# Performance work log

Hardware: AMD Instinct MI355X
Metric: run time of the kernel (lower is better)

## Reference

```python
import jax, jax.numpy as jnp
import numpy as np
from jax import lax

B = 128
ROUTING_ITER = 3
EPS = 1e-9


def _conv(x, w, b, stride):
    y = lax.conv_general_dilated(x, w, window_strides=(stride, stride), padding='VALID',
                                 dimension_numbers=('NCHW', 'OIHW', 'NCHW'))
    return y + b[None, :, None, None]


def _squash(s):
    # squash along capsule dim (axis=3), s: [B,1,10,16,1]
    sq = jnp.sum(s * s, axis=3, keepdims=True)
    return (sq / (1.0 + sq)) * s / jnp.sqrt(sq + EPS)


def setup_inputs() -> dict:
    key = jax.random.key(0)
    ks = jax.random.split(key, 16)
    x = jax.random.normal(ks[0], (B, 1, 28, 28), dtype=jnp.float32)
    labels = jax.random.randint(ks[1], (B,), 0, 10)
    y = jax.nn.one_hot(labels, 10, dtype=jnp.float32)
    conv1_w = jax.random.normal(ks[2], (256, 1, 9, 9), dtype=jnp.float32) * 0.05
    conv1_b = jnp.zeros((256,), dtype=jnp.float32)
    caps1_w = jax.random.normal(ks[3], (256, 256, 9, 9), dtype=jnp.float32) * 0.01
    caps1_b = jnp.zeros((256,), dtype=jnp.float32)
    W = jax.random.normal(ks[4], (1, 1152, 10, 8, 16), dtype=jnp.float32) * 0.05
    caps_bias = jnp.zeros((1, 1, 10, 16, 1), dtype=jnp.float32)
    fc1_w = jax.random.normal(ks[5], (512, 16), dtype=jnp.float32) * 0.1
    fc1_b = jnp.zeros((512,), dtype=jnp.float32)
    fc2_w = jax.random.normal(ks[6], (1024, 512), dtype=jnp.float32) * 0.04
    fc2_b = jnp.zeros((1024,), dtype=jnp.float32)
    fc3_w = jax.random.normal(ks[7], (784, 1024), dtype=jnp.float32) * 0.03
    fc3_b = jnp.zeros((784,), dtype=jnp.float32)
    return {'x': x, 'y': y, 'conv1_w': conv1_w, 'conv1_b': conv1_b,
            'caps1_w': caps1_w, 'caps1_b': caps1_b, 'W': W, 'caps_bias': caps_bias,
            'fc1_w': fc1_w, 'fc1_b': fc1_b, 'fc2_w': fc2_w, 'fc2_b': fc2_b,
            'fc3_w': fc3_w, 'fc3_b': fc3_b}


def _forward(x, y, conv1_w, conv1_b, caps1_w, caps1_b, W, caps_bias,
             fc1_w, fc1_b, fc2_w, fc2_b, fc3_w, fc3_b):
    h = jax.nn.relu(_conv(x, conv1_w, conv1_b, 1))          # [B,256,20,20]
    h = jax.nn.relu(_conv(h, caps1_w, caps1_b, 2))          # [B,256,6,6]

    # faithful repeat+view layout from the torch code (NOT a transpose)
    x_view = jnp.tile(h.reshape(B, 256, 1, 6, 6), (1, 1, 10, 1, 1)).reshape(B, 1152, 10, 8, 1)
    W_view = jnp.broadcast_to(W, (B, 1152, 10, 8, 16)).reshape(B, 1152, 10, 16, 8)
    u_hat = jnp.matmul(W_view, x_view)                      # [B,1152,10,16,1]
    u_hat_stopped = lax.stop_gradient(u_hat)

    b_ij = jnp.zeros((B, 1152, 10, 1, 1), dtype=u_hat.dtype)
    V_J = None
    for r in range(ROUTING_ITER):
        c_ij = jax.nn.softmax(b_ij, axis=2)                 # softmax over 10 classes
        if r < ROUTING_ITER - 1:
            s_j = jnp.sum(c_ij * u_hat_stopped, axis=1, keepdims=True) + caps_bias
            v_j = _squash(s_j)                              # [B,1,10,16,1]
            # agreement: u_hat^T . v, [B,1152,10,1,16] @ [B,1152,10,16,1]
            agree = jnp.matmul(u_hat_stopped.reshape(B, 1152, 10, 1, 16),
                               jnp.broadcast_to(v_j, (B, 1152, 10, 16, 1)))
            b_ij = b_ij + agree
        else:
            s_j = jnp.sum(c_ij * u_hat, axis=1, keepdims=True) + caps_bias
            V_J = _squash(s_j)                              # [B,1,10,16,1]

    caps_out = jnp.squeeze(V_J, axis=1)                     # [B,10,16,1]
    v_length = jnp.sqrt(jnp.sum(caps_out * caps_out, axis=2, keepdims=True) + EPS)
    v_length = v_length.reshape(B, 10, 1, 1)

    # torch: squeeze -> [B,10,16], then .view(B,16,10) (reshape, not transpose)
    flat = caps_out.reshape(B, 10, 16).reshape(B, 16, 10)
    masked_v = jnp.matmul(flat, y.reshape(B, 10, 1)).reshape(B, 16)

    fc1 = masked_v @ fc1_w.T + fc1_b                        # no activation (faithful)
    fc2 = fc1 @ fc2_w.T + fc2_b
    reconstruction = jax.nn.sigmoid(fc2 @ fc3_w.T + fc3_b)  # [B,784]
    return v_length, reconstruction


def reference(x, y, conv1_w, conv1_b, caps1_w, caps1_b, W, caps_bias,
              fc1_w, fc1_b, fc2_w, fc2_b, fc3_w, fc3_b):
    return _forward(x, y, conv1_w, conv1_b, caps1_w, caps1_b, W, caps_bias,
                    fc1_w, fc1_b, fc2_w, fc2_b, fc3_w, fc3_b)
```

## Files before the change

### kernel.cpp

```cpp
#include <hip/hip_runtime.h>
#include <hip/hip_bf16.h>

typedef unsigned short ushort_t;
typedef __attribute__((ext_vector_type(8))) short short8;
typedef __attribute__((ext_vector_type(4))) float f32x4;


#define OFFB_H1T  0u
#define OFFB_WT   26214400u
#define OFFB_PART 36831232u
#define OFFB_H2   55705600u
#define OFFB_UH   60424192u
#define OFFB_BIJ  107610112u
#define OFFB_C    113508352u
#define OFFB_V    119406592u
#define OFFB_F1   119488512u
#define OFFB_F2   119750656u

__device__ __forceinline__ ushort_t f2bf(float f) {
  union { float f; unsigned int u; } c; c.f = f;
  unsigned int r = (c.u + 0x7FFFu + ((c.u >> 16) & 1u)) >> 16;
  return (ushort_t)r;
}
__device__ __forceinline__ float bf2f(ushort_t u) {
  union { unsigned int i; float f; } c; c.i = ((unsigned int)u) << 16;
  return c.f;
}

__global__ __launch_bounds__(256) void conv1_kernel(
    const float* __restrict__ x, const float* __restrict__ w,
    const float* __restrict__ bias, ushort_t* __restrict__ h1t) {
  int blk = blockIdx.x;
  int b = blk / 20, oy = blk % 20;
  int co = threadIdx.x;
  __shared__ float xs[252];
  for (int l = co; l < 252; l += 256)
    xs[l] = x[b * 784 + (oy + l / 28) * 28 + (l % 28)];
  __syncthreads();
  float bs = bias[co];
  float acc[20];
#pragma unroll
  for (int i = 0; i < 20; ++i) acc[i] = bs;
  for (int ky = 0; ky < 9; ++ky) {
    float xr[28];
#pragma unroll
    for (int i = 0; i < 28; ++i) xr[i] = xs[ky * 28 + i];
    float wk[9];
#pragma unroll
    for (int kx = 0; kx < 9; ++kx) wk[kx] = w[co * 81 + ky * 9 + kx];
#pragma unroll
    for (int kx = 0; kx < 9; ++kx)
#pragma unroll
      for (int ox = 0; ox < 20; ++ox) acc[ox] += wk[kx] * xr[ox + kx];
  }
  int xb = (b * 20 + oy) * 20;
#pragma unroll
  for (int ox = 0; ox < 20; ++ox)
    h1t[(xb + ox) * 256 + co] = f2bf(fmaxf(acc[ox], 0.f));
}

__global__ __launch_bounds__(256) void wreorder_kernel(
    const float* __restrict__ w, ushort_t* __restrict__ wt) {
  int co = blockIdx.x;
  __shared__ ushort_t wl[256 * 82];
  int t = threadIdx.x;
  const float* src = w + (size_t)co * 20736;
  for (int e = t; e < 20736; e += 256) {
    int ci = e / 81, kk = e - ci * 81;
    wl[ci * 82 + kk] = f2bf(src[e]);
  }
  __syncthreads();
  for (int kk = 0; kk < 81; ++kk)
    wt[((size_t)kk * 256 + co) * 256 + t] = wl[t * 82 + kk];
}

__global__ __launch_bounds__(256) void caps1_gemm(
    const ushort_t* __restrict__ h1t, const ushort_t* __restrict__ wt,
    float* __restrict__ part) {
  int blk = blockIdx.x;
  int chunk = blk / 288;
  int tile = blk - chunk * 288;
  int gm0 = (tile >> 2) * 64;
  int gn0 = (tile & 3) * 64;
  int ks0 = chunk * 81, ks1 = ks0 + 81;
  int t = threadIdx.x;
  int wave = t >> 6, lane = t & 63;
  int wm = (wave >> 1) * 32, wn = (wave & 1) * 32;
  int lr = lane & 15, lg = lane >> 4;

  __shared__ __align__(16) ushort_t As[2][64 * 72];
  __shared__ __align__(16) ushort_t Bs[2][64 * 72];

  int r = t >> 2, seg = t & 3;
  int m = gm0 + r;
  int b = m / 36, pos = m - b * 36;
  int oy = pos / 6, ox = pos - oy * 6;
  const ushort_t* arow = h1t + ((b * 20 + 2 * oy) * 20 + 2 * ox) * 256 + seg * 16;
  const ushort_t* brow = wt + (gn0 + r) * 256 + seg * 16;
  int lds_off = r * 72 + seg * 16;

  f32x4 acc[2][2];
#pragma unroll
  for (int i = 0; i < 2; ++i)
#pragma unroll
    for (int j = 0; j < 2; ++j)
#pragma unroll
      for (int e = 0; e < 4; ++e) acc[i][j][e] = 0.f;

  float4 ra0, ra1, rb0, rb1;
  {
    int kk = ks0 >> 2, ci0 = (ks0 & 3) << 6;
    int ky = kk / 9, kx = kk - ky * 9;
    const ushort_t* ap = arow + (ky * 20 + kx) * 256 + ci0;
    ra0 = *(const float4*)(ap);
    ra1 = *(const float4*)(ap + 8);
    const ushort_t* bp = brow + kk * 65536 + ci0;
    rb0 = *(const float4*)(bp);
    rb1 = *(const float4*)(bp + 8);
  }
  *(float4*)&As[0][lds_off] = ra0;
  *(float4*)&As[0][lds_off + 8] = ra1;
  *(float4*)&Bs[0][lds_off] = rb0;
  *(float4*)&Bs[0][lds_off + 8] = rb1;
  __syncthreads();

  int buf = 0;
  for (int ks = ks0; ks < ks1; ++ks) {
    int nxt = ks + 1;
    if (nxt < ks1) {
      int kk = nxt >> 2, ci0 = (nxt & 3) << 6;
      int ky = kk / 9, kx = kk - ky * 9;
      const ushort_t* ap = arow + (ky * 20 + kx) * 256 + ci0;
      ra0 = *(const float4*)(ap);
      ra1 = *(const float4*)(ap + 8);
      const ushort_t* bp = brow + kk * 65536 + ci0;
      rb0 = *(const float4*)(bp);
      rb1 = *(const float4*)(bp + 8);
    }
    short8 af[2][2], bfr[2][2];
#pragma unroll
    for (int kh = 0; kh < 2; ++kh) {
#pragma unroll
      for (int mf = 0; mf < 2; ++mf)
        af[mf][kh] = *(const short8*)&As[buf][(wm + mf * 16 + lr) * 72 + kh * 32 + lg * 8];
#pragma unroll
      for (int nf = 0; nf < 2; ++nf)
        bfr[nf][kh] = *(const short8*)&Bs[buf][(wn + nf * 16 + lr) * 72 + kh * 32 + lg * 8];
    }
#pragma unroll
    for (int kh = 0; kh < 2; ++kh)
#pragma unroll
      for (int mf = 0; mf < 2; ++mf)
#pragma unroll
        for (int nf = 0; nf < 2; ++nf)
          acc[mf][nf] = __builtin_amdgcn_mfma_f32_16x16x32_bf16(
              af[mf][kh], bfr[nf][kh], acc[mf][nf], 0, 0, 0);
    __syncthreads();
    if (nxt < ks1) {
      int nb = buf ^ 1;
      *(float4*)&As[nb][lds_off] = ra0;
      *(float4*)&As[nb][lds_off + 8] = ra1;
      *(float4*)&Bs[nb][lds_off] = rb0;
      *(float4*)&Bs[nb][lds_off + 8] = rb1;
      __syncthreads();
    }
    buf ^= 1;
  }

#pragma unroll
  for (int mf = 0; mf < 2; ++mf)
#pragma unroll
    for (int nf = 0; nf < 2; ++nf) {
      int nn = gn0 + wn + nf * 16 + lr;
#pragma unroll
      for (int reg = 0; reg < 4; ++reg) {
        int mm = gm0 + wm + mf * 16 + lg * 4 + reg;
        part[((size_t)chunk * 4608 + mm) * 256 + nn] = acc[mf][nf][reg];
      }
    }
}

__global__ __launch_bounds__(256) void reduce_kernel(
    const float* __restrict__ part, const float* __restrict__ bias,
    float* __restrict__ h2) {
  int m = blockIdx.x;
  int n = threadIdx.x;
  size_t o = (size_t)m * 256 + n;
  float s = part[o] + part[o + 4608 * 256] + part[o + 2 * 4608 * 256] +
            part[o + 3 * 4608 * 256];
  h2[o] = fmaxf(s + bias[n], 0.f);
}

__global__ __launch_bounds__(256) void uhat_kernel(
    const float* __restrict__ h2, const float* __restrict__ W,
    ushort_t* __restrict__ uh) {
  int blk = blockIdx.x;
  int bh = blk & 1;
  int qpc = blk >> 1;
  int q = qpc / 72;
  int pc = qpc - q * 72;
  int p0 = pc * 16;
  int b0 = bh * 64;
  __shared__ float Wl[16][132];
  __shared__ float xl[64][16][9];
  int t = threadIdx.x;
#pragma unroll
  for (int it = 0; it < 2; ++it) {
    int idx = t * 2 + it;
    int row = idx >> 5;
    int c4 = idx & 31;
    float4 vv = *(reinterpret_cast<const float4*>(
        &W[(size_t)((p0 + row) * 10 + q) * 128]) + c4);
    Wl[row][c4 * 4 + 0] = vv.x;
    Wl[row][c4 * 4 + 1] = vv.y;
    Wl[row][c4 * 4 + 2] = vv.z;
    Wl[row][c4 * 4 + 3] = vv.w;
  }
  for (int j = 0; j < 32; ++j) {
    int e = t + 256 * j;
    int b_l = e >> 7;
    int rem = e & 127;
    int i = rem >> 3, n = rem & 7;
    int f = (p0 + i) * 80 + q * 8 + n;
    xl[b_l][i][n] = h2[((size_t)(b0 + b_l) * 36 + (f % 36)) * 256 + (f / 360)];
  }
  __syncthreads();
  int p_l = t & 15;
  int b_ll = t >> 4;
  const float* wr = &Wl[p_l][0];
#pragma unroll
  for (int k = 0; k < 4; ++k) {
    int b_l = b_ll + 16 * k;
    float xv[8];
#pragma unroll
    for (int n = 0; n < 8; ++n) xv[n] = xl[b_l][p_l][n];
    short8 o0, o1;
#pragma unroll
    for (int a = 0; a < 8; ++a) {
      float ue = 0.f, uo = 0.f;
#pragma unroll
      for (int n = 0; n < 8; ++n) {
        ue += wr[a * 16 + n] * xv[n];
        uo += wr[a * 16 + 8 + n] * xv[n];
      }
      if (a < 4) { o0[2 * a] = (short)f2bf(ue); o0[2 * a + 1] = (short)f2bf(uo); }
      else { o1[2 * (a - 4)] = (short)f2bf(ue); o1[2 * (a - 4) + 1] = (short)f2bf(uo); }
    }
    size_t dst = ((size_t)((b0 + b_l) * 10 + q) * 1152 + p0 + p_l) * 16;
    *(short8*)&uh[dst] = o0;
    *(short8*)&uh[dst + 8] = o1;
  }
}

template <int MODE>
__global__ __launch_bounds__(64) void sv_kernel(
    const ushort_t* __restrict__ uh, const float* __restrict__ cbuf,
    const float* __restrict__ caps_bias, float* __restrict__ v,
    float* __restrict__ out) {
  int bq = blockIdx.x;
  int q = bq % 10;
  int t = threadIdx.x;
  const ushort_t* ub = &uh[(size_t)bq * 1152 * 16];
  const float* cb = &cbuf[(size_t)bq * 1152];
  float s[16];
#pragma unroll
  for (int m = 0; m < 16; ++m) s[m] = 0.f;
  for (int p = t; p < 1152; p += 64) {
    short8 u0 = *(const short8*)&ub[p * 16];
    short8 u1 = *(const short8*)&ub[p * 16 + 8];
    float c = (MODE == 0) ? 0.1f : cb[p];
#pragma unroll
    for (int m = 0; m < 8; ++m) s[m] += c * bf2f((ushort_t)u0[m]);
#pragma unroll
    for (int m = 0; m < 8; ++m) s[8 + m] += c * bf2f((ushort_t)u1[m]);
  }
#pragma unroll
  for (int m = 0; m < 16; ++m) {
    float val = s[m];
#pragma unroll
    for (int off = 32; off > 0; off >>= 1) val += __shfl_down(val, off);
    s[m] = val;
  }
  if (t == 0) {
    float sq = 0.f;
#pragma unroll
    for (int m = 0; m < 16; ++m) {
      s[m] += caps_bias[q * 16 + m];
      sq += s[m] * s[m];
    }
    float coef = (sq / (1.f + sq)) * rsqrtf(sq + 1e-9f);
    float vl2 = 0.f;
#pragma unroll
    for (int m = 0; m < 16; ++m) {
      float vv = coef * s[m];
      v[bq * 16 + m] = vv;
      vl2 += vv * vv;
    }
    if (MODE == 2) out[bq] = sqrtf(vl2 + 1e-9f);
  }
}

template <bool FIRST>
__global__ __launch_bounds__(256) void agree_kernel(
    const ushort_t* __restrict__ uh, const float* __restrict__ v,
    float* __restrict__ bij, float* __restrict__ cbuf) {
  int tid = blockIdx.x * 256 + threadIdx.x;
  int b = tid / 1152;
  int p = tid - b * 1152;
  float br[10];
  float* bp = &bij[(size_t)tid * 10];
#pragma unroll
  for (int q = 0; q < 10; ++q) {
    const ushort_t* ub = &uh[(size_t)((b * 10 + q) * 1152 + p) * 16];
    short8 u0 = *(const short8*)ub;
    short8 u1 = *(const short8*)(ub + 8);
    const float4* v4 = reinterpret_cast<const float4*>(&v[(b * 10 + q) * 16]);
    float4 b0 = v4[0], b1 = v4[1], b2 = v4[2], b3 = v4[3];
    float d = bf2f((ushort_t)u0[0]) * b0.x + bf2f((ushort_t)u0[1]) * b0.y
            + bf2f((ushort_t)u0[2]) * b0.z + bf2f((ushort_t)u0[3]) * b0.w
            + bf2f((ushort_t)u0[4]) * b1.x + bf2f((ushort_t)u0[5]) * b1.y
            + bf2f((ushort_t)u0[6]) * b1.z + bf2f((ushort_t)u0[7]) * b1.w
            + bf2f((ushort_t)u1[0]) * b2.x + bf2f((ushort_t)u1[1]) * b2.y
            + bf2f((ushort_t)u1[2]) * b2.z + bf2f((ushort_t)u1[3]) * b2.w
            + bf2f((ushort_t)u1[4]) * b3.x + bf2f((ushort_t)u1[5]) * b3.y
            + bf2f((ushort_t)u1[6]) * b3.z + bf2f((ushort_t)u1[7]) * b3.w;
    br[q] = (FIRST ? 0.f : bp[q]) + d;
  }
  float mx = br[0];
#pragma unroll
  for (int q = 1; q < 10; ++q) mx = fmaxf(mx, br[q]);
  float den = 0.f;
  float ex[10];
#pragma unroll
  for (int q = 0; q < 10; ++q) { ex[q] = __expf(br[q] - mx); den += ex[q]; }
  float inv = 1.f / den;
#pragma unroll
  for (int q = 0; q < 10; ++q) {
    bp[q] = br[q];
    cbuf[(size_t)(b * 10 + q) * 1152 + p] = ex[q] * inv;
  }
}

__global__ __launch_bounds__(128) void fc1_kernel(
    const float* __restrict__ v, const float* __restrict__ y,
    const float* __restrict__ fc1_w, const float* __restrict__ fc1_b,
    float* __restrict__ f1g) {
  int b = blockIdx.x, t = threadIdx.x;
  __shared__ float mv[16];
  if (t < 16) {
    const float* vb = &v[b * 160];
    float a = 0.f;
#pragma unroll
    for (int tt = 0; tt < 10; ++tt) a += vb[t * 10 + tt] * y[b * 10 + tt];
    mv[t] = a;
  }
  __syncthreads();
  for (int o = t; o < 512; o += 128) {
    const float4* wr = reinterpret_cast<const float4*>(&fc1_w[o * 16]);
    float4 w0 = wr[0], w1 = wr[1], w2 = wr[2], w3 = wr[3];
    f1g[b * 512 + o] = fc1_b[o]
        + mv[0] * w0.x + mv[1] * w0.y + mv[2] * w0.z + mv[3] * w0.w
        + mv[4] * w1.x + mv[5] * w1.y + mv[6] * w1.z + mv[7] * w1.w
        + mv[8] * w2.x + mv[9] * w2.y + mv[10] * w2.z + mv[11] * w2.w
        + mv[12] * w3.x + mv[13] * w3.y + mv[14] * w3.z + mv[15] * w3.w;
  }
}

__global__ __launch_bounds__(256) void fc2_kernel(
    const float* __restrict__ f1g, const float* __restrict__ fc2_w,
    const float* __restrict__ fc2_b, float* __restrict__ f2g) {
  int b = blockIdx.x >> 2;
  int o = (blockIdx.x & 3) * 256 + threadIdx.x;
  __shared__ float f1[512];
  for (int l = threadIdx.x; l < 512; l += 256) f1[l] = f1g[b * 512 + l];
  __syncthreads();
  const float4* wr = reinterpret_cast<const float4*>(&fc2_w[o * 512]);
  float a = fc2_b[o];
#pragma unroll 4
  for (int k4 = 0; k4 < 128; ++k4) {
    float4 w4 = wr[k4];
    a += f1[4 * k4] * w4.x + f1[4 * k4 + 1] * w4.y + f1[4 * k4 + 2] * w4.z +
         f1[4 * k4 + 3] * w4.w;
  }
  f2g[b * 1024 + o] = a;
}

__global__ __launch_bounds__(256) void fc3_kernel(
    const float* __restrict__ f2g, const float* __restrict__ fc3_w,
    const float* __restrict__ fc3_b, float* __restrict__ out) {
  int b = blockIdx.x >> 2;
  int oc = (blockIdx.x & 3) * 196;
  __shared__ float f2[1024];
  for (int l = threadIdx.x; l < 1024; l += 256) f2[l] = f2g[b * 1024 + l];
  __syncthreads();
  if (threadIdx.x >= 196) return;
  int o = oc + threadIdx.x;
  const float4* wr = reinterpret_cast<const float4*>(&fc3_w[o * 1024]);
  float a = fc3_b[o];
#pragma unroll 4
  for (int k4 = 0; k4 < 256; ++k4) {
    float4 w4 = wr[k4];
    a += f2[4 * k4] * w4.x + f2[4 * k4 + 1] * w4.y + f2[4 * k4 + 2] * w4.z +
         f2[4 * k4 + 3] * w4.w;
  }
  out[1280 + b * 784 + o] = 1.f / (1.f + __expf(-a));
}

extern "C" void kernel_launch(void* const* d_in, const int* in_sizes, int n_in,
                              void* d_out, int out_size, void* d_ws, size_t ws_size,
                              hipStream_t stream) {
  const float* x       = (const float*)d_in[0];
  const float* y       = (const float*)d_in[1];
  const float* conv1_w = (const float*)d_in[2];
  const float* conv1_b = (const float*)d_in[3];
  const float* caps1_w = (const float*)d_in[4];
  const float* caps1_b = (const float*)d_in[5];
  const float* W       = (const float*)d_in[6];
  const float* cbias   = (const float*)d_in[7];
  const float* fc1_w   = (const float*)d_in[8];
  const float* fc1_b   = (const float*)d_in[9];
  const float* fc2_w   = (const float*)d_in[10];
  const float* fc2_b   = (const float*)d_in[11];
  const float* fc3_w   = (const float*)d_in[12];
  const float* fc3_b   = (const float*)d_in[13];
  float* out = (float*)d_out;

  char* wsb = (char*)d_ws;
  ushort_t* h1t  = (ushort_t*)(wsb + OFFB_H1T);
  ushort_t* wt   = (ushort_t*)(wsb + OFFB_WT);
  float*    part = (float*)(wsb + OFFB_PART);
  float*    h2   = (float*)(wsb + OFFB_H2);
  ushort_t* uh   = (ushort_t*)(wsb + OFFB_UH);
  float*    bij  = (float*)(wsb + OFFB_BIJ);
  float*    c    = (float*)(wsb + OFFB_C);
  float*    v    = (float*)(wsb + OFFB_V);
  float*    f1   = (float*)(wsb + OFFB_F1);
  float*    f2   = (float*)(wsb + OFFB_F2);

  conv1_kernel<<<2560, 256, 0, stream>>>(x, conv1_w, conv1_b, h1t);
  wreorder_kernel<<<256, 256, 0, stream>>>(caps1_w, wt);
  caps1_gemm<<<1152, 256, 0, stream>>>(h1t, wt, part);
  reduce_kernel<<<4608, 256, 0, stream>>>(part, caps1_b, h2);
  uhat_kernel<<<1440, 256, 0, stream>>>(h2, W, uh);

  sv_kernel<0><<<1280, 64, 0, stream>>>(uh, c, cbias, v, out);
  agree_kernel<true><<<576, 256, 0, stream>>>(uh, v, bij, c);
  sv_kernel<1><<<1280, 64, 0, stream>>>(uh, c, cbias, v, out);
  agree_kernel<false><<<576, 256, 0, stream>>>(uh, v, bij, c);
  sv_kernel<2><<<1280, 64, 0, stream>>>(uh, c, cbias, v, out);

  fc1_kernel<<<128, 128, 0, stream>>>(v, y, fc1_w, fc1_b, f1);
  fc2_kernel<<<512, 256, 0, stream>>>(f1, fc2_w, fc2_b, f2);
  fc3_kernel<<<512, 256, 0, stream>>>(f2, fc3_w, fc3_b, out);
}
```

Baseline: 341.9 us.

## Split caps1 GEMM K by channel slice, XOR-swizzle LDS, remap block order

Each split-K chunk now owns a fixed 64-channel slice and iterates over all 81 kernel positions, replacing the earlier contiguous K-range split. The padded 72-element LDS rows become 64-element rows with an XOR swizzle to avoid bank conflicts, which reduces LDS footprint. Block indices are permuted so that consecutive blocks, likely spread across XCDs, share input tiles for better L2 locality. The partial-sum output layout stays the same, so the downstream reduction is unchanged.

```diff
diff --git a/kernel.cpp b/kernel.cpp
--- a/kernel.cpp
+++ b/kernel.cpp
@@ -77,27 +77,32 @@
 __global__ __launch_bounds__(256) void caps1_gemm(
     const ushort_t* __restrict__ h1t, const ushort_t* __restrict__ wt,
     float* __restrict__ part) {
-  int blk = blockIdx.x;
-  int chunk = blk / 288;
-  int tile = blk - chunk * 288;
+  int lb = (blockIdx.x & 7) * 144 + (blockIdx.x >> 3);
+  int chunk = lb / 288;
+  int tile = lb - chunk * 288;
   int gm0 = (tile >> 2) * 64;
   int gn0 = (tile & 3) * 64;
-  int ks0 = chunk * 81, ks1 = ks0 + 81;
+  int ci0 = chunk << 6;
   int t = threadIdx.x;
   int wave = t >> 6, lane = t & 63;
   int wm = (wave >> 1) * 32, wn = (wave & 1) * 32;
   int lr = lane & 15, lg = lane >> 4;
 
-  __shared__ __align__(16) ushort_t As[2][64 * 72];
-  __shared__ __align__(16) ushort_t Bs[2][64 * 72];
+  __shared__ __align__(16) ushort_t As[2][64 * 64];
+  __shared__ __align__(16) ushort_t Bs[2][64 * 64];
 
   int r = t >> 2, seg = t & 3;
   int m = gm0 + r;
   int b = m / 36, pos = m - b * 36;
   int oy = pos / 6, ox = pos - oy * 6;
-  const ushort_t* arow = h1t + ((b * 20 + 2 * oy) * 20 + 2 * ox) * 256 + seg * 16;
-  const ushort_t* brow = wt + (gn0 + r) * 256 + seg * 16;
-  int lds_off = r * 72 + seg * 16;
+  const ushort_t* arow = h1t + ((b * 20 + 2 * oy) * 20 + 2 * ox) * 256 + ci0 + seg * 16;
+  const ushort_t* brow = wt + (gn0 + r) * 256 + ci0 + seg * 16;
+  int rx = r & 7;
+  int st0 = r * 64 + (((seg << 1) | 0) ^ rx) * 8;
+  int st1 = r * 64 + (((seg << 1) | 1) ^ rx) * 8;
+  int lx = lr & 7;
+  int sl0 = ((0 * 4 + lg) ^ lx) * 8;
+  int sl1 = ((1 * 4 + lg) ^ lx) * 8;
 
   f32x4 acc[2][2];
 #pragma unroll
@@ -108,44 +113,40 @@
       for (int e = 0; e < 4; ++e) acc[i][j][e] = 0.f;
 
   float4 ra0, ra1, rb0, rb1;
-  {
-    int kk = ks0 >> 2, ci0 = (ks0 & 3) << 6;
-    int ky = kk / 9, kx = kk - ky * 9;
-    const ushort_t* ap = arow + (ky * 20 + kx) * 256 + ci0;
-    ra0 = *(const float4*)(ap);
-    ra1 = *(const float4*)(ap + 8);
-    const ushort_t* bp = brow + kk * 65536 + ci0;
-    rb0 = *(const float4*)(bp);
-    rb1 = *(const float4*)(bp + 8);
-  }
-  *(float4*)&As[0][lds_off] = ra0;
-  *(float4*)&As[0][lds_off + 8] = ra1;
-  *(float4*)&Bs[0][lds_off] = rb0;
-  *(float4*)&Bs[0][lds_off + 8] = rb1;
+  ra0 = *(const float4*)(arow);
+  ra1 = *(const float4*)(arow + 8);
+  rb0 = *(const float4*)(brow);
+  rb1 = *(const float4*)(brow + 8);
+  *(float4*)&As[0][st0] = ra0;
+  *(float4*)&As[0][st1] = ra1;
+  *(float4*)&Bs[0][st0] = rb0;
+  *(float4*)&Bs[0][st1] = rb1;
   __syncthreads();
 
   int buf = 0;
-  for (int ks = ks0; ks < ks1; ++ks) {
-    int nxt = ks + 1;
-    if (nxt < ks1) {
-      int kk = nxt >> 2, ci0 = (nxt & 3) << 6;
-      int ky = kk / 9, kx = kk - ky * 9;
-      const ushort_t* ap = arow + (ky * 20 + kx) * 256 + ci0;
+  for (int kk = 0; kk < 81; ++kk) {
+    int nxt = kk + 1;
+    if (nxt < 81) {
+      int ky = nxt / 9, kx = nxt - ky * 9;
+      const ushort_t* ap = arow + (ky * 20 + kx) * 256;
       ra0 = *(const float4*)(ap);
       ra1 = *(const float4*)(ap + 8);
-      const ushort_t* bp = brow + kk * 65536 + ci0;
+      const ushort_t* bp = brow + nxt * 65536;
       rb0 = *(const float4*)(bp);
       rb1 = *(const float4*)(bp + 8);
     }
     short8 af[2][2], bfr[2][2];
 #pragma unroll
-    for (int kh = 0; kh < 2; ++kh) {
-#pragma unroll
-      for (int mf = 0; mf < 2; ++mf)
-        af[mf][kh] = *(const short8*)&As[buf][(wm + mf * 16 + lr) * 72 + kh * 32 + lg * 8];
-#pragma unroll
-      for (int nf = 0; nf < 2; ++nf)
-        bfr[nf][kh] = *(const short8*)&Bs[buf][(wn + nf * 16 + lr) * 72 + kh * 32 + lg * 8];
+    for (int mf = 0; mf < 2; ++mf) {
+      int ra = (wm + mf * 16 + lr) * 64;
+      af[mf][0] = *(const short8*)&As[buf][ra + sl0];
+      af[mf][1] = *(const short8*)&As[buf][ra + sl1];
+    }
+#pragma unroll
+    for (int nf = 0; nf < 2; ++nf) {
+      int rb = (wn + nf * 16 + lr) * 64;
+      bfr[nf][0] = *(const short8*)&Bs[buf][rb + sl0];
+      bfr[nf][1] = *(const short8*)&Bs[buf][rb + sl1];
     }
 #pragma unroll
     for (int kh = 0; kh < 2; ++kh)
@@ -156,12 +157,12 @@
           acc[mf][nf] = __builtin_amdgcn_mfma_f32_16x16x32_bf16(
               af[mf][kh], bfr[nf][kh], acc[mf][nf], 0, 0, 0);
     __syncthreads();
-    if (nxt < ks1) {
+    if (nxt < 81) {
       int nb = buf ^ 1;
-      *(float4*)&As[nb][lds_off] = ra0;
-      *(float4*)&As[nb][lds_off + 8] = ra1;
-      *(float4*)&Bs[nb][lds_off] = rb0;
-      *(float4*)&Bs[nb][lds_off + 8] = rb1;
+      *(float4*)&As[nb][st0] = ra0;
+      *(float4*)&As[nb][st1] = ra1;
+      *(float4*)&Bs[nb][st0] = rb0;
+      *(float4*)&Bs[nb][st1] = rb1;
       __syncthreads();
     }
     buf ^= 1;
```

New measurement: 327.3 us. 1.04x faster.
